# Optimization experiments

Measured on AMD Instinct MI355X. Metric: run time of the kernel, lower is better.

Reference implementation:

```python
import jax, jax.numpy as jnp
import numpy as np
import math

B, S, D, H = 2, 2048, 1024, 16
DK = D // H

def setup_inputs() -> dict:
    key = jax.random.key(0)
    ks = jax.random.split(key, 12)
    def xavier(k, shape):
        fan_in, fan_out = shape[1], shape[0]
        limit = math.sqrt(6.0 / (fan_in + fan_out))
        return jax.random.uniform(k, shape, jnp.float32, -limit, limit)
    inp = {
        'query': jax.random.normal(ks[0], (B, S, D), jnp.float32),
        'key':   jax.random.normal(ks[1], (B, S, D), jnp.float32),
        'value': jax.random.normal(ks[2], (B, S, D), jnp.float32),
        # causal mask, broadcast over heads: (B, 1, S, S), 1 = keep, 0 = mask
        'mask':  jnp.broadcast_to(jnp.tril(jnp.ones((S, S), jnp.int32)), (B, 1, S, S)),
        'Wq': xavier(ks[3], (D, D)), 'bq': jnp.zeros((D,), jnp.float32),
        'Wk': xavier(ks[4], (D, D)), 'bk': jnp.zeros((D,), jnp.float32),
        'Wv': xavier(ks[5], (D, D)), 'bv': jnp.zeros((D,), jnp.float32),
        'Wo': xavier(ks[6], (D, D)), 'bo': jnp.zeros((D,), jnp.float32),
    }
    return inp

def _split_heads(x):
    # (B, S, D) -> (B, H, S, DK)
    b, s, _ = x.shape
    return x.reshape(b, s, H, DK).transpose(0, 2, 1, 3)

def reference(query, key, value, mask, Wq, bq, Wk, bk, Wv, bv, Wo, bo):
    # torch nn.Linear: y = x @ W.T + b
    Q = _split_heads(query @ Wq.T + bq)   # (B,H,S,DK)
    K = _split_heads(key   @ Wk.T + bk)
    V = _split_heads(value @ Wv.T + bv)
    scores = jnp.einsum('bhqd,bhkd->bhqk', Q, K) / math.sqrt(DK)  # (B,H,S,S)
    scores = jnp.where(mask == 0, jnp.float32(-1e9), scores)
    attn = jax.nn.softmax(scores, axis=-1)  # dropout p=0 -> identity
    out = jnp.einsum('bhqk,bhkd->bhqd', attn, V)  # (B,H,S,DK)
    out = out.transpose(0, 2, 1, 3).reshape(query.shape[0], query.shape[1], D)
    return out @ Wo.T + bo
```

## Files before the change

kernel.cpp:

```cpp
#include <hip/hip_runtime.h>
#include <hip/hip_bf16.h>
#include <type_traits>


typedef __attribute__((ext_vector_type(8))) short short8;
typedef __attribute__((ext_vector_type(4))) short s16x4;
typedef __attribute__((ext_vector_type(4))) float floatx4;

__device__ __forceinline__ short f2bf(float x) {
    union { float f; unsigned u; } v; v.f = x;
    unsigned r = v.u + 0x7fffu + ((v.u >> 16) & 1u);
    return (short)(r >> 16);
}

__device__ __forceinline__ unsigned pk2bf(float a, float b) {
    union { __hip_bfloat162 h2; unsigned u; } cv;
    cv.h2 = __float22bfloat162_rn(make_float2(a, b));
    return cv.u;
}

__device__ __forceinline__ float fast_exp2(float x) {
#if __has_builtin(__builtin_amdgcn_exp2f)
    return __builtin_amdgcn_exp2f(x);
#else
    return __expf(x * 0.69314718056f);
#endif
}

typedef __attribute__((address_space(3))) short lds_short;
typedef __attribute__((address_space(1))) const short glb_short;
__device__ __forceinline__ void load_lds16(const void* g, void* l) {
    __builtin_amdgcn_global_load_lds((glb_short*)g, (lds_short*)l, 16, 0, 0);
}

__global__ __launch_bounds__(256) void cvt_all(
        const float* __restrict__ q, const float* __restrict__ k,
        const float* __restrict__ v,
        const float* __restrict__ wq, const float* __restrict__ wk,
        const float* __restrict__ wv, const float* __restrict__ wo,
        unsigned short* __restrict__ xq, unsigned short* __restrict__ xk,
        unsigned short* __restrict__ xv,
        unsigned short* __restrict__ wqb, unsigned short* __restrict__ wkb,
        unsigned short* __restrict__ wvb, unsigned short* __restrict__ wob) {
    const float* s; unsigned short* d;
    int bx = blockIdx.x;
    switch (blockIdx.y) {
        case 0: s = q; d = xq; break;
        case 1: s = k; d = xk; break;
        case 2: s = v; d = xv; break;
        default: {
            int wsel = bx >> 9; bx &= 511;
            s = (wsel == 0) ? wq : (wsel == 1) ? wk : (wsel == 2) ? wv : wo;
            d = (wsel == 0) ? wqb : (wsel == 1) ? wkb : (wsel == 2) ? wvb : wob;
        }
    }
    size_t i = ((size_t)bx * 256 + threadIdx.x) * 8;
    floatx4 a = *(const floatx4*)(s + i), b2 = *(const floatx4*)(s + i + 4);
    union { unsigned u[4]; short8 v8; } o;
    o.u[0] = pk2bf(a[0], a[1]);  o.u[1] = pk2bf(a[2], a[3]);
    o.u[2] = pk2bf(b2[0], b2[1]); o.u[3] = pk2bf(b2[2], b2[3]);
    *(short8*)(d + i) = o.v8;
}

__global__ __launch_bounds__(256) void gemm_qkv(
        const unsigned short* __restrict__ Xq, const unsigned short* __restrict__ Xk,
        const unsigned short* __restrict__ Xv,
        const unsigned short* __restrict__ Wq, const unsigned short* __restrict__ Wk,
        const unsigned short* __restrict__ Wv,
        const float* __restrict__ bq, const float* __restrict__ bk,
        const float* __restrict__ bv,
        unsigned short* __restrict__ Qb, unsigned short* __restrict__ Kb,
        unsigned short* __restrict__ Vb) {
    constexpr int K = 1024, N = 1024;
    __shared__ short As[128 * 64];
    __shared__ short Bs[128 * 64];
    const int t = threadIdx.x;
    const int chunk = blockIdx.y >> 5, my = blockIdx.y & 31;
    const unsigned short* A = chunk == 0 ? Xq : chunk == 1 ? Xk : Xv;
    const unsigned short* W = chunk == 0 ? Wq : chunk == 1 ? Wk : Wv;
    const float* bias        = chunk == 0 ? bq : chunk == 1 ? bk : bv;
    unsigned short* Y        = chunk == 0 ? Qb : chunk == 1 ? Kb : Vb;
    const float scale = chunk == 0 ? 0.1803368801f : 1.0f;
    const int m0 = my * 128, n0 = blockIdx.x * 128;
    const int lane = t & 63, w = t >> 6;
    const int l16 = lane & 15, quad = lane >> 4;
    const int wm = w >> 1, wn = w & 1;
    const int srow8 = t >> 3, scs8 = t & 7;
    floatx4 acc[4][4] = {};

    for (int k0 = 0; k0 < K; k0 += 64) {
        __syncthreads();
        for (int i = 0; i < 4; i++) {
            const int row = i * 32 + srow8;
            const int cg = scs8 ^ (row & 7);
            load_lds16(A + (size_t)(m0 + row) * K + k0 + cg * 8, &As[i * 2048 + t * 8]);
            load_lds16(W + (size_t)(n0 + row) * K + k0 + cg * 8, &Bs[i * 2048 + t * 8]);
        }
        __syncthreads();

        for (int kc = 0; kc < 2; kc++) {
            short8 af[4], bf[4];
            for (int ms = 0; ms < 4; ms++) {
                const int row = wm * 64 + ms * 16 + l16;
                af[ms] = *(short8*)&As[row * 64 + (((kc << 2) | quad) ^ (row & 7)) * 8];
            }
            for (int ns = 0; ns < 4; ns++) {
                const int row = wn * 64 + ns * 16 + l16;
                bf[ns] = *(short8*)&Bs[row * 64 + (((kc << 2) | quad) ^ (row & 7)) * 8];
            }
            for (int ms = 0; ms < 4; ms++)
                for (int ns = 0; ns < 4; ns++)
                    acc[ms][ns] = __builtin_amdgcn_mfma_f32_16x16x32_bf16(
                            af[ms], bf[ns], acc[ms][ns], 0, 0, 0);
        }
    }

    for (int ms = 0; ms < 4; ms++)
        for (int ns = 0; ns < 4; ns++) {
            int col = n0 + wn * 64 + ns * 16 + l16;
            float bb = bias[col];
            for (int r = 0; r < 4; r++) {
                int row = m0 + wm * 64 + ms * 16 + quad * 4 + r;
                Y[(size_t)row * N + col] =
                    (unsigned short)f2bf((acc[ms][ns][r] + bb) * scale);
            }
        }
}

__global__ __launch_bounds__(256) void gemm_o(
        const unsigned short* __restrict__ A, const unsigned short* __restrict__ W,
        float* __restrict__ P) {
    constexpr int K = 1024, N = 1024;
    __shared__ short As[128 * 64];
    __shared__ short Bs[128 * 64];
    const int t = threadIdx.x;
    const int m0 = blockIdx.y * 128, n0 = blockIdx.x * 128;
    const int kz = blockIdx.z;
    const int lane = t & 63, w = t >> 6;
    const int l16 = lane & 15, quad = lane >> 4;
    const int wm = w >> 1, wn = w & 1;
    const int srow8 = t >> 3, scs8 = t & 7;
    floatx4 acc[4][4] = {};

    for (int k0 = kz * 512; k0 < kz * 512 + 512; k0 += 64) {
        __syncthreads();
        for (int i = 0; i < 4; i++) {
            const int row = i * 32 + srow8;
            const int cg = scs8 ^ (row & 7);
            load_lds16(A + (size_t)(m0 + row) * K + k0 + cg * 8, &As[i * 2048 + t * 8]);
            load_lds16(W + (size_t)(n0 + row) * K + k0 + cg * 8, &Bs[i * 2048 + t * 8]);
        }
        __syncthreads();

        for (int kc = 0; kc < 2; kc++) {
            short8 af[4], bf[4];
            for (int ms = 0; ms < 4; ms++) {
                const int row = wm * 64 + ms * 16 + l16;
                af[ms] = *(short8*)&As[row * 64 + (((kc << 2) | quad) ^ (row & 7)) * 8];
            }
            for (int ns = 0; ns < 4; ns++) {
                const int row = wn * 64 + ns * 16 + l16;
                bf[ns] = *(short8*)&Bs[row * 64 + (((kc << 2) | quad) ^ (row & 7)) * 8];
            }
            for (int ms = 0; ms < 4; ms++)
                for (int ns = 0; ns < 4; ns++)
                    acc[ms][ns] = __builtin_amdgcn_mfma_f32_16x16x32_bf16(
                            af[ms], bf[ns], acc[ms][ns], 0, 0, 0);
        }
    }

    float* Pz = P + (size_t)kz * 4096 * N;
    for (int ms = 0; ms < 4; ms++)
        for (int ns = 0; ns < 4; ns++) {
            int col = n0 + wn * 64 + ns * 16 + l16;
            for (int r = 0; r < 4; r++) {
                int row = m0 + wm * 64 + ms * 16 + quad * 4 + r;
                Pz[(size_t)row * N + col] = acc[ms][ns][r];
            }
        }
}

__global__ __launch_bounds__(256) void reduce_o(const float* __restrict__ P,
        const float* __restrict__ bo, float* __restrict__ out) {
    size_t i = ((size_t)blockIdx.x * 256 + threadIdx.x) * 4;
    floatx4 a = *(const floatx4*)(P + i);
    floatx4 b = *(const floatx4*)(P + (size_t)4096 * 1024 + i);
    floatx4 bb = *(const floatx4*)(bo + (i & 1023));
    *(floatx4*)(out + i) = a + b + bb;
}

__global__ __launch_bounds__(256) void attn_kernel(
        const unsigned short* __restrict__ Q, const unsigned short* __restrict__ Kp,
        const unsigned short* __restrict__ Vp, unsigned short* __restrict__ O) {
    __shared__ short Ks[64 * 72];
    __shared__ short Vt[64 * 72];
    __shared__ short PsA[4][16 * 70];
    __shared__ short PsB[4][16 * 70];
    const int t = threadIdx.x;
    const int bx = blockIdx.x;
    const int unit = bx & 15, h = (bx >> 4) & 15, b = bx >> 8;
    const int q0A = unit * 64, q0B = (31 - unit) * 64;
    const int lane = t & 63, w = t >> 6, l16 = lane & 15, quad = lane >> 4;
    const int krow = t >> 2, kcg = (t & 3) * 16;
    const int vp2 = t & 31, vg = t >> 5;

    short8 qfA[2], qfB[2];
    {
        const size_t baseA = ((size_t)(b * 2048 + q0A + w * 16 + l16)) * 1024 + h * 64;
        qfA[0] = *(const short8*)(Q + baseA + quad * 8);
        qfA[1] = *(const short8*)(Q + baseA + 32 + quad * 8);
        const size_t baseB = ((size_t)(b * 2048 + q0B + w * 16 + l16)) * 1024 + h * 64;
        qfB[0] = *(const short8*)(Q + baseB + quad * 8);
        qfB[1] = *(const short8*)(Q + baseB + 32 + quad * 8);
    }
    float lA = 0.f, lB = 0.f;
    floatx4 oA[4] = {}, oB[4] = {};

    short8 ka, kb, va, vc;
    {
        const size_t kbse = ((size_t)(b * 2048 + krow)) * 1024 + h * 64 + kcg;
        ka = *(const short8*)(Kp + kbse);
        kb = *(const short8*)(Kp + kbse + 8);
        const size_t vbse = ((size_t)(b * 2048 + 2 * vp2)) * 1024 + h * 64 + vg * 8;
        va = *(const short8*)(Vp + vbse);
        vc = *(const short8*)(Vp + vbse + 1024);
    }

    for (int kv0 = 0; kv0 < q0B + 64; kv0 += 64) {
        __syncthreads();
        *(short8*)&Ks[krow * 72 + kcg] = ka;
        *(short8*)&Ks[krow * 72 + kcg + 8] = kb;
        for (int i = 0; i < 8; i++) {
            unsigned pk = (unsigned)(unsigned short)va[i] |
                          ((unsigned)(unsigned short)vc[i] << 16);
            *(unsigned*)&Vt[(vg * 8 + i) * 72 + 2 * vp2] = pk;
        }
        __syncthreads();

        if (kv0 < q0B) {
            const size_t kbse = ((size_t)(b * 2048 + kv0 + 64 + krow)) * 1024 + h * 64 + kcg;
            ka = *(const short8*)(Kp + kbse);
            kb = *(const short8*)(Kp + kbse + 8);
            const size_t vbse = ((size_t)(b * 2048 + kv0 + 64 + 2 * vp2)) * 1024 + h * 64 + vg * 8;
            va = *(const short8*)(Vp + vbse);
            vc = *(const short8*)(Vp + vbse + 1024);
        }

        auto body = [&](auto dual_c) {
            constexpr bool DUAL = decltype(dual_c)::value;
            floatx4 sB[4] = {};
            floatx4 sA[4];
            if constexpr (DUAL)
                for (int i = 0; i < 4; i++) sA[i] = (floatx4){0.f, 0.f, 0.f, 0.f};
            for (int hh = 0; hh < 4; hh++)
                for (int kc = 0; kc < 2; kc++) {
                    short8 kf = *(short8*)&Ks[(hh * 16 + l16) * 72 + kc * 32 + quad * 8];
                    sB[hh] = __builtin_amdgcn_mfma_f32_16x16x32_bf16(kf, qfB[kc], sB[hh], 0, 0, 0);
                    if constexpr (DUAL)
                        sA[hh] = __builtin_amdgcn_mfma_f32_16x16x32_bf16(kf, qfA[kc], sA[hh], 0, 0, 0);
                }

            {
                const bool needmask = (kv0 + 63 > q0B + w * 16);
                const int qg = q0B + w * 16 + l16;
                float ls = 0.f;
                for (int hh = 0; hh < 4; hh++) {
                    float p[4];
                    for (int r = 0; r < 4; r++) {
                        int kv = kv0 + hh * 16 + quad * 4 + r;
                        float e = fast_exp2(sB[hh][r]);
                        p[r] = (needmask && kv > qg) ? 0.f : e;
                        ls += p[r];
                    }
                    union { unsigned u[2]; s16x4 v4; } pw;
                    pw.u[0] = pk2bf(p[0], p[1]); pw.u[1] = pk2bf(p[2], p[3]);
                    *(s16x4*)&PsB[w][l16 * 70 + hh * 16 + quad * 4] = pw.v4;
                }
                ls += __shfl_xor(ls, 16);
                ls += __shfl_xor(ls, 32);
                lB += ls;
            }
            if constexpr (DUAL) {
                const bool needmask = (kv0 + 63 > q0A + w * 16);
                const int qg = q0A + w * 16 + l16;
                float ls = 0.f;
                for (int hh = 0; hh < 4; hh++) {
                    float p[4];
                    for (int r = 0; r < 4; r++) {
                        int kv = kv0 + hh * 16 + quad * 4 + r;
                        float e = fast_exp2(sA[hh][r]);
                        p[r] = (needmask && kv > qg) ? 0.f : e;
                        ls += p[r];
                    }
                    union { unsigned u[2]; s16x4 v4; } pw;
                    pw.u[0] = pk2bf(p[0], p[1]); pw.u[1] = pk2bf(p[2], p[3]);
                    *(s16x4*)&PsA[w][l16 * 70 + hh * 16 + quad * 4] = pw.v4;
                }
                ls += __shfl_xor(ls, 16);
                ls += __shfl_xor(ls, 32);
                lA += ls;
            }

            short8 pB0 = *(short8*)&PsB[w][l16 * 70 + quad * 8];
            short8 pB1 = *(short8*)&PsB[w][l16 * 70 + 32 + quad * 8];
            short8 pA0, pA1;
            if constexpr (DUAL) {
                pA0 = *(short8*)&PsA[w][l16 * 70 + quad * 8];
                pA1 = *(short8*)&PsA[w][l16 * 70 + 32 + quad * 8];
            }
            for (int nc = 0; nc < 4; nc++) {
                short8 vf0 = *(short8*)&Vt[(nc * 16 + l16) * 72 + quad * 8];
                short8 vf1 = *(short8*)&Vt[(nc * 16 + l16) * 72 + 32 + quad * 8];
                oB[nc] = __builtin_amdgcn_mfma_f32_16x16x32_bf16(vf0, pB0, oB[nc], 0, 0, 0);
                oB[nc] = __builtin_amdgcn_mfma_f32_16x16x32_bf16(vf1, pB1, oB[nc], 0, 0, 0);
                if constexpr (DUAL) {
                    oA[nc] = __builtin_amdgcn_mfma_f32_16x16x32_bf16(vf0, pA0, oA[nc], 0, 0, 0);
                    oA[nc] = __builtin_amdgcn_mfma_f32_16x16x32_bf16(vf1, pA1, oA[nc], 0, 0, 0);
                }
            }
        };
        if (kv0 <= q0A) body(std::integral_constant<bool, true>{});
        else            body(std::integral_constant<bool, false>{});
    }

    {
        const float rl = 1.f / lB;
        const size_t orow = ((size_t)(b * 2048 + q0B + w * 16 + l16)) * 1024 + h * 64;
        for (int nc = 0; nc < 4; nc++) {
            union { unsigned u[2]; s16x4 v4; } ow;
            ow.u[0] = pk2bf(oB[nc][0] * rl, oB[nc][1] * rl);
            ow.u[1] = pk2bf(oB[nc][2] * rl, oB[nc][3] * rl);
            *(s16x4*)(O + orow + nc * 16 + quad * 4) = ow.v4;
        }
    }
    {
        const float rl = 1.f / lA;
        const size_t orow = ((size_t)(b * 2048 + q0A + w * 16 + l16)) * 1024 + h * 64;
        for (int nc = 0; nc < 4; nc++) {
            union { unsigned u[2]; s16x4 v4; } ow;
            ow.u[0] = pk2bf(oA[nc][0] * rl, oA[nc][1] * rl);
            ow.u[1] = pk2bf(oA[nc][2] * rl, oA[nc][3] * rl);
            *(s16x4*)(O + orow + nc * 16 + quad * 4) = ow.v4;
        }
    }
}

extern "C" void kernel_launch(void* const* d_in, const int* in_sizes, int n_in,
                              void* d_out, int out_size, void* d_ws, size_t ws_size,
                              hipStream_t stream) {
    const float* query = (const float*)d_in[0];
    const float* key   = (const float*)d_in[1];
    const float* value = (const float*)d_in[2];
    const float* Wq = (const float*)d_in[4];
    const float* bq = (const float*)d_in[5];
    const float* Wk = (const float*)d_in[6];
    const float* bk = (const float*)d_in[7];
    const float* Wv = (const float*)d_in[8];
    const float* bv = (const float*)d_in[9];
    const float* Wo = (const float*)d_in[10];
    const float* bo = (const float*)d_in[11];

    const size_t NE = (size_t)4096 * 1024;
    const size_t WE = (size_t)1024 * 1024;
    unsigned short* Xq  = (unsigned short*)d_ws;
    unsigned short* Xk  = Xq + NE;
    unsigned short* Xv  = Xk + NE;
    unsigned short* Qb  = Xv + NE;
    unsigned short* Kb  = Qb + NE;
    unsigned short* Vb  = Kb + NE;
    unsigned short* Ob  = Vb + NE;
    unsigned short* Wqb = Ob + NE;
    unsigned short* Wkb = Wqb + WE;
    unsigned short* Wvb = Wkb + WE;
    unsigned short* Wob = Wvb + WE;
    float* Opart = (float*)d_ws;

    cvt_all<<<dim3(2048, 4), 256, 0, stream>>>(query, key, value, Wq, Wk, Wv, Wo,
                                               Xq, Xk, Xv, Wqb, Wkb, Wvb, Wob);
    gemm_qkv<<<dim3(8, 96), 256, 0, stream>>>(Xq, Xk, Xv, Wqb, Wkb, Wvb,
                                              bq, bk, bv, Qb, Kb, Vb);
    attn_kernel<<<dim3(512), 256, 0, stream>>>(Qb, Kb, Vb, Ob);
    gemm_o<<<dim3(8, 32, 2), 256, 0, stream>>>(Ob, Wob, Opart);
    reduce_o<<<dim3(4096), 256, 0, stream>>>(Opart, bo, (float*)d_out);
}
```

Baseline: 258.7 us.

## Split paired attention blocks into single-tile blocks and drop split-K output GEMM

The attention kernel no longer pairs a short and a long query tile per block. It launches 1024 single-tile blocks, ordered so the longest causal rows go first, which trades K/V reuse across the pair for more parallelism and simpler code. The output projection drops the split-K partials and the separate reduce kernel. It uses 128x64 tiles over the full K and adds the bias directly, avoiding the fp32 partial write and re-read and one launch. The risk is less K/V sharing per block and smaller GEMM tiles.

```diff
diff --git a/kernel.cpp b/kernel.cpp
--- a/kernel.cpp
+++ b/kernel.cpp
@@ -129,64 +129,58 @@
 
 __global__ __launch_bounds__(256) void gemm_o(
         const unsigned short* __restrict__ A, const unsigned short* __restrict__ W,
-        float* __restrict__ P) {
+        const float* __restrict__ bo, float* __restrict__ out) {
     constexpr int K = 1024, N = 1024;
     __shared__ short As[128 * 64];
-    __shared__ short Bs[128 * 64];
+    __shared__ short Bs[64 * 64];
     const int t = threadIdx.x;
-    const int m0 = blockIdx.y * 128, n0 = blockIdx.x * 128;
-    const int kz = blockIdx.z;
+    const int m0 = blockIdx.y * 128, n0 = blockIdx.x * 64;
     const int lane = t & 63, w = t >> 6;
     const int l16 = lane & 15, quad = lane >> 4;
     const int wm = w >> 1, wn = w & 1;
     const int srow8 = t >> 3, scs8 = t & 7;
-    floatx4 acc[4][4] = {};
-
-    for (int k0 = kz * 512; k0 < kz * 512 + 512; k0 += 64) {
+    floatx4 acc[4][2] = {};
+
+    for (int k0 = 0; k0 < K; k0 += 64) {
         __syncthreads();
         for (int i = 0; i < 4; i++) {
             const int row = i * 32 + srow8;
             const int cg = scs8 ^ (row & 7);
             load_lds16(A + (size_t)(m0 + row) * K + k0 + cg * 8, &As[i * 2048 + t * 8]);
+        }
+        for (int i = 0; i < 2; i++) {
+            const int row = i * 32 + srow8;
+            const int cg = scs8 ^ (row & 7);
             load_lds16(W + (size_t)(n0 + row) * K + k0 + cg * 8, &Bs[i * 2048 + t * 8]);
         }
         __syncthreads();
 
         for (int kc = 0; kc < 2; kc++) {
-            short8 af[4], bf[4];
+            short8 af[4], bf[2];
             for (int ms = 0; ms < 4; ms++) {
                 const int row = wm * 64 + ms * 16 + l16;
                 af[ms] = *(short8*)&As[row * 64 + (((kc << 2) | quad) ^ (row & 7)) * 8];
             }
-            for (int ns = 0; ns < 4; ns++) {
-                const int row = wn * 64 + ns * 16 + l16;
+            for (int ns = 0; ns < 2; ns++) {
+                const int row = wn * 32 + ns * 16 + l16;
                 bf[ns] = *(short8*)&Bs[row * 64 + (((kc << 2) | quad) ^ (row & 7)) * 8];
             }
             for (int ms = 0; ms < 4; ms++)
-                for (int ns = 0; ns < 4; ns++)
+                for (int ns = 0; ns < 2; ns++)
                     acc[ms][ns] = __builtin_amdgcn_mfma_f32_16x16x32_bf16(
                             af[ms], bf[ns], acc[ms][ns], 0, 0, 0);
         }
     }
 
-    float* Pz = P + (size_t)kz * 4096 * N;
     for (int ms = 0; ms < 4; ms++)
-        for (int ns = 0; ns < 4; ns++) {
-            int col = n0 + wn * 64 + ns * 16 + l16;
+        for (int ns = 0; ns < 2; ns++) {
+            int col = n0 + wn * 32 + ns * 16 + l16;
+            float bb = bo[col];
             for (int r = 0; r < 4; r++) {
                 int row = m0 + wm * 64 + ms * 16 + quad * 4 + r;
-                Pz[(size_t)row * N + col] = acc[ms][ns][r];
-            }
-        }
-}
-
-__global__ __launch_bounds__(256) void reduce_o(const float* __restrict__ P,
-        const float* __restrict__ bo, float* __restrict__ out) {
-    size_t i = ((size_t)blockIdx.x * 256 + threadIdx.x) * 4;
-    floatx4 a = *(const floatx4*)(P + i);
-    floatx4 b = *(const floatx4*)(P + (size_t)4096 * 1024 + i);
-    floatx4 bb = *(const floatx4*)(bo + (i & 1023));
-    *(floatx4*)(out + i) = a + b + bb;
+                out[(size_t)row * N + col] = acc[ms][ns][r] + bb;
+            }
+        }
 }
 
 __global__ __launch_bounds__(256) void attn_kernel(
@@ -194,27 +188,25 @@
         const unsigned short* __restrict__ Vp, unsigned short* __restrict__ O) {
     __shared__ short Ks[64 * 72];
     __shared__ short Vt[64 * 72];
-    __shared__ short PsA[4][16 * 70];
-    __shared__ short PsB[4][16 * 70];
+    __shared__ short Ps[4][16 * 72];
     const int t = threadIdx.x;
     const int bx = blockIdx.x;
-    const int unit = bx & 15, h = (bx >> 4) & 15, b = bx >> 8;
-    const int q0A = unit * 64, q0B = (31 - unit) * 64;
+    const int s = bx & 511, half = bx >> 9;
+    const int p = s & 15, h = (s >> 4) & 15, b = s >> 8;
+    const int unit = half ? p : (31 - p);
+    const int q0 = unit * 64;
     const int lane = t & 63, w = t >> 6, l16 = lane & 15, quad = lane >> 4;
     const int krow = t >> 2, kcg = (t & 3) * 16;
     const int vp2 = t & 31, vg = t >> 5;
 
-    short8 qfA[2], qfB[2];
+    short8 qf[2];
     {
-        const size_t baseA = ((size_t)(b * 2048 + q0A + w * 16 + l16)) * 1024 + h * 64;
-        qfA[0] = *(const short8*)(Q + baseA + quad * 8);
-        qfA[1] = *(const short8*)(Q + baseA + 32 + quad * 8);
-        const size_t baseB = ((size_t)(b * 2048 + q0B + w * 16 + l16)) * 1024 + h * 64;
-        qfB[0] = *(const short8*)(Q + baseB + quad * 8);
-        qfB[1] = *(const short8*)(Q + baseB + 32 + quad * 8);
-    }
-    float lA = 0.f, lB = 0.f;
-    floatx4 oA[4] = {}, oB[4] = {};
+        const size_t base = ((size_t)(b * 2048 + q0 + w * 16 + l16)) * 1024 + h * 64;
+        qf[0] = *(const short8*)(Q + base + quad * 8);
+        qf[1] = *(const short8*)(Q + base + 32 + quad * 8);
+    }
+    float l = 0.f;
+    floatx4 o[4] = {};
 
     short8 ka, kb, va, vc;
     {
@@ -226,7 +218,7 @@
         vc = *(const short8*)(Vp + vbse + 1024);
     }
 
-    for (int kv0 = 0; kv0 < q0B + 64; kv0 += 64) {
+    for (int kv0 = 0; kv0 <= q0; kv0 += 64) {
         __syncthreads();
         *(short8*)&Ks[krow * 72 + kcg] = ka;
         *(short8*)&Ks[krow * 72 + kcg + 8] = kb;
@@ -237,7 +229,7 @@
         }
         __syncthreads();
 
-        if (kv0 < q0B) {
+        if (kv0 < q0) {
             const size_t kbse = ((size_t)(b * 2048 + kv0 + 64 + krow)) * 1024 + h * 64 + kcg;
             ka = *(const short8*)(Kp + kbse);
             kb = *(const short8*)(Kp + kbse + 8);
@@ -246,102 +238,51 @@
             vc = *(const short8*)(Vp + vbse + 1024);
         }
 
-        auto body = [&](auto dual_c) {
-            constexpr bool DUAL = decltype(dual_c)::value;
-            floatx4 sB[4] = {};
-            floatx4 sA[4];
-            if constexpr (DUAL)
-                for (int i = 0; i < 4; i++) sA[i] = (floatx4){0.f, 0.f, 0.f, 0.f};
-            for (int hh = 0; hh < 4; hh++)
-                for (int kc = 0; kc < 2; kc++) {
-                    short8 kf = *(short8*)&Ks[(hh * 16 + l16) * 72 + kc * 32 + quad * 8];
-                    sB[hh] = __builtin_amdgcn_mfma_f32_16x16x32_bf16(kf, qfB[kc], sB[hh], 0, 0, 0);
-                    if constexpr (DUAL)
-                        sA[hh] = __builtin_amdgcn_mfma_f32_16x16x32_bf16(kf, qfA[kc], sA[hh], 0, 0, 0);
+        floatx4 sv[4] = {};
+        for (int hh = 0; hh < 4; hh++)
+            for (int kc = 0; kc < 2; kc++) {
+                short8 kf = *(short8*)&Ks[(hh * 16 + l16) * 72 + kc * 32 + quad * 8];
+                sv[hh] = __builtin_amdgcn_mfma_f32_16x16x32_bf16(kf, qf[kc], sv[hh], 0, 0, 0);
+            }
+
+        {
+            const bool needmask = (kv0 + 63 > q0 + w * 16);
+            const int qg = q0 + w * 16 + l16;
+            float ls = 0.f;
+            for (int hh = 0; hh < 4; hh++) {
+                float pv[4];
+                for (int r = 0; r < 4; r++) {
+                    int kv = kv0 + hh * 16 + quad * 4 + r;
+                    float e = fast_exp2(sv[hh][r]);
+                    pv[r] = (needmask && kv > qg) ? 0.f : e;
+                    ls += pv[r];
                 }
-
-            {
-                const bool needmask = (kv0 + 63 > q0B + w * 16);
-                const int qg = q0B + w * 16 + l16;
-                float ls = 0.f;
-                for (int hh = 0; hh < 4; hh++) {
-                    float p[4];
-                    for (int r = 0; r < 4; r++) {
-                        int kv = kv0 + hh * 16 + quad * 4 + r;
-                        float e = fast_exp2(sB[hh][r]);
-                        p[r] = (needmask && kv > qg) ? 0.f : e;
-                        ls += p[r];
-                    }
-                    union { unsigned u[2]; s16x4 v4; } pw;
-                    pw.u[0] = pk2bf(p[0], p[1]); pw.u[1] = pk2bf(p[2], p[3]);
-                    *(s16x4*)&PsB[w][l16 * 70 + hh * 16 + quad * 4] = pw.v4;
-                }
-                ls += __shfl_xor(ls, 16);
-                ls += __shfl_xor(ls, 32);
-                lB += ls;
-            }
-            if constexpr (DUAL) {
-                const bool needmask = (kv0 + 63 > q0A + w * 16);
-                const int qg = q0A + w * 16 + l16;
-                float ls = 0.f;
-                for (int hh = 0; hh < 4; hh++) {
-                    float p[4];
-                    for (int r = 0; r < 4; r++) {
-                        int kv = kv0 + hh * 16 + quad * 4 + r;
-                        float e = fast_exp2(sA[hh][r]);
-                        p[r] = (needmask && kv > qg) ? 0.f : e;
-                        ls += p[r];
-                    }
-                    union { unsigned u[2]; s16x4 v4; } pw;
-                    pw.u[0] = pk2bf(p[0], p[1]); pw.u[1] = pk2bf(p[2], p[3]);
-                    *(s16x4*)&PsA[w][l16 * 70 + hh * 16 + quad * 4] = pw.v4;
-                }
-                ls += __shfl_xor(ls, 16);
-                ls += __shfl_xor(ls, 32);
-                lA += ls;
-            }
-
-            short8 pB0 = *(short8*)&PsB[w][l16 * 70 + quad * 8];
-            short8 pB1 = *(short8*)&PsB[w][l16 * 70 + 32 + quad * 8];
-            short8 pA0, pA1;
-            if constexpr (DUAL) {
-                pA0 = *(short8*)&PsA[w][l16 * 70 + quad * 8];
-                pA1 = *(short8*)&PsA[w][l16 * 70 + 32 + quad * 8];
-            }
-            for (int nc = 0; nc < 4; nc++) {
-                short8 vf0 = *(short8*)&Vt[(nc * 16 + l16) * 72 + quad * 8];
-                short8 vf1 = *(short8*)&Vt[(nc * 16 + l16) * 72 + 32 + quad * 8];
-                oB[nc] = __builtin_amdgcn_mfma_f32_16x16x32_bf16(vf0, pB0, oB[nc], 0, 0, 0);
-                oB[nc] = __builtin_amdgcn_mfma_f32_16x16x32_bf16(vf1, pB1, oB[nc], 0, 0, 0);
-                if constexpr (DUAL) {
-                    oA[nc] = __builtin_amdgcn_mfma_f32_16x16x32_bf16(vf0, pA0, oA[nc], 0, 0, 0);
-                    oA[nc] = __builtin_amdgcn_mfma_f32_16x16x32_bf16(vf1, pA1, oA[nc], 0, 0, 0);
-                }
-            }
-        };
-        if (kv0 <= q0A) body(std::integral_constant<bool, true>{});
-        else            body(std::integral_constant<bool, false>{});
-    }
-
-    {
-        const float rl = 1.f / lB;
-        const size_t orow = ((size_t)(b * 2048 + q0B + w * 16 + l16)) * 1024 + h * 64;
+                union { unsigned u[2]; s16x4 v4; } pw;
+                pw.u[0] = pk2bf(pv[0], pv[1]); pw.u[1] = pk2bf(pv[2], pv[3]);
+                *(s16x4*)&Ps[w][l16 * 72 + hh * 16 + quad * 4] = pw.v4;
+            }
+            ls += __shfl_xor(ls, 16);
+            ls += __shfl_xor(ls, 32);
+            l += ls;
+        }
+
+        short8 p0 = *(short8*)&Ps[w][l16 * 72 + quad * 8];
+        short8 p1 = *(short8*)&Ps[w][l16 * 72 + 32 + quad * 8];
         for (int nc = 0; nc < 4; nc++) {
-            union { unsigned u[2]; s16x4 v4; } ow;
-            ow.u[0] = pk2bf(oB[nc][0] * rl, oB[nc][1] * rl);
-            ow.u[1] = pk2bf(oB[nc][2] * rl, oB[nc][3] * rl);
-            *(s16x4*)(O + orow + nc * 16 + quad * 4) = ow.v4;
-        }
-    }
-    {
-        const float rl = 1.f / lA;
-        const size_t orow = ((size_t)(b * 2048 + q0A + w * 16 + l16)) * 1024 + h * 64;
-        for (int nc = 0; nc < 4; nc++) {
-            union { unsigned u[2]; s16x4 v4; } ow;
-            ow.u[0] = pk2bf(oA[nc][0] * rl, oA[nc][1] * rl);
-            ow.u[1] = pk2bf(oA[nc][2] * rl, oA[nc][3] * rl);
-            *(s16x4*)(O + orow + nc * 16 + quad * 4) = ow.v4;
-        }
+            short8 vf0 = *(short8*)&Vt[(nc * 16 + l16) * 72 + quad * 8];
+            short8 vf1 = *(short8*)&Vt[(nc * 16 + l16) * 72 + 32 + quad * 8];
+            o[nc] = __builtin_amdgcn_mfma_f32_16x16x32_bf16(vf0, p0, o[nc], 0, 0, 0);
+            o[nc] = __builtin_amdgcn_mfma_f32_16x16x32_bf16(vf1, p1, o[nc], 0, 0, 0);
+        }
+    }
+
+    const float rl = 1.f / l;
+    const size_t orow = ((size_t)(b * 2048 + q0 + w * 16 + l16)) * 1024 + h * 64;
+    for (int nc = 0; nc < 4; nc++) {
+        union { unsigned u[2]; s16x4 v4; } ow;
+        ow.u[0] = pk2bf(o[nc][0] * rl, o[nc][1] * rl);
+        ow.u[1] = pk2bf(o[nc][2] * rl, o[nc][3] * rl);
+        *(s16x4*)(O + orow + nc * 16 + quad * 4) = ow.v4;
     }
 }
 
@@ -373,13 +314,11 @@
     unsigned short* Wkb = Wqb + WE;
     unsigned short* Wvb = Wkb + WE;
     unsigned short* Wob = Wvb + WE;
-    float* Opart = (float*)d_ws;
 
     cvt_all<<<dim3(2048, 4), 256, 0, stream>>>(query, key, value, Wq, Wk, Wv, Wo,
                                                Xq, Xk, Xv, Wqb, Wkb, Wvb, Wob);
     gemm_qkv<<<dim3(8, 96), 256, 0, stream>>>(Xq, Xk, Xv, Wqb, Wkb, Wvb,
                                               bq, bk, bv, Qb, Kb, Vb);
-    attn_kernel<<<dim3(512), 256, 0, stream>>>(Qb, Kb, Vb, Ob);
-    gemm_o<<<dim3(8, 32, 2), 256, 0, stream>>>(Ob, Wob, Opart);
-    reduce_o<<<dim3(4096), 256, 0, stream>>>(Opart, bo, (float*)d_out);
-}
+    attn_kernel<<<dim3(1024), 256, 0, stream>>>(Qb, Kb, Vb, Ob);
+    gemm_o<<<dim3(16, 32), 256, 0, stream>>>(Ob, Wob, bo, (float*)d_out);
+}
```

Measured after the change: 245.0 us. 1.06x faster.
